# Kernel optimization log

Measured on AMD Instinct MI355X. Metric: run time of the kernel, lower is better.

Reference implementation:

```python
import jax, jax.numpy as jnp
import numpy as np

H = 128; B = 2
NG = 20000; NP = 3000
E_GG = 200000; E_TG = 200000; E_GP = 200000; E_PP = 100000
TAU_TG = 0.5; TOPK_TG = 16; TAU_GP = 0.5; TOPK_GP = 32
SQRT_H = float(np.sqrt(H))


def _mlp(x, w1, b1, w2, b2):
    # build_mlp(H, [H], H): Linear -> ReLU -> Linear (dropout=0)
    return jax.nn.relu(x @ w1 + b1) @ w2 + b2


def _scatter_sum(msgs, dst, num):
    # msgs: [B, E, H] -> [B, num, H]
    b, _, h = msgs.shape
    return jnp.zeros((b, num, h), msgs.dtype).at[:, dst, :].add(msgs)


def _prune(scores, dst, topk, tau):
    # per-target top-k + threshold pruning; scores [B, E], dst [E]
    E = scores.shape[1]
    pos = jnp.arange(E)
    def one(s):
        order = jnp.lexsort((-s, dst))  # primary: dst asc, secondary: score desc
        d_sorted = dst[order]
        is_start = jnp.concatenate([jnp.ones((1,), bool), d_sorted[1:] != d_sorted[:-1]])
        seg_start = jax.lax.associative_scan(jnp.maximum, jnp.where(is_start, pos, 0))
        rank = pos - seg_start  # rank within segment (0 = largest score)
        keep_sorted = (rank < topk) & (s[order] > tau)
        keep = jnp.zeros((E,), bool).at[order].set(keep_sorted)
        return jnp.where(keep, s, 0.0)
    return jax.vmap(one)(scores)


def _forward(gene_states, pathway_states, gg_w, tg_w, gp_w, pp_w,
             mlp_gg_w1, mlp_gg_b1, mlp_gg_w2, mlp_gg_b2,
             mlp_gp_w1, mlp_gp_b1, mlp_gp_w2, mlp_gp_b2,
             mlp_pp_w1, mlp_pp_b1, mlp_pp_w2, mlp_pp_b2,
             mlp_pg_w1, mlp_pg_b1, mlp_pg_w2, mlp_pg_b2,
             w_gg, w_pp, w_pg,
             tg_q, tg_k, tg_v_tf, tg_v_gene,
             gp_q, gp_k, gp_v,
             gg_src, gg_dst, tg_src, tg_dst, gp_src, gp_dst, pp_src, pp_dst):
    # Layer 1: gene-gene message passing with fixed edge weights
    gg_msgs = (gene_states[:, gg_src, :] @ w_gg) * gg_w[None, :, None]
    h1 = _mlp(gene_states, mlp_gg_w1, mlp_gg_b1, mlp_gg_w2, mlp_gg_b2) + _scatter_sum(gg_msgs, gg_dst, NG)

    # Layer 2: TF->gene attention with per-target pruning
    q_gene = h1 @ tg_q; k_tf = h1 @ tg_k; v_tf = h1 @ tg_v_tf; v_gene = h1 @ tg_v_gene
    raw_tg = jnp.einsum('beh,beh->be', q_gene[:, tg_dst, :], k_tf[:, tg_src, :]) / SQRT_H
    tg_scores = jax.nn.sigmoid(raw_tg * tg_w[None, :])
    tg_sel = _prune(tg_scores, tg_dst, TOPK_TG, TAU_TG)
    h2 = v_gene + _scatter_sum(tg_sel[..., None] * v_tf[:, tg_src, :], tg_dst, NG)

    # Layer 3: gene->pathway attention with pruning
    q_p = pathway_states @ gp_q; k_g = h2 @ gp_k; v_g = h2 @ gp_v
    raw_gp = jnp.einsum('beh,beh->be', q_p[:, gp_dst, :], k_g[:, gp_src, :]) / SQRT_H
    gp_scores = jax.nn.sigmoid(raw_gp * gp_w[None, :])
    gp_sel = _prune(gp_scores, gp_dst, TOPK_GP, TAU_GP)
    bar_h3 = _mlp(pathway_states, mlp_gp_w1, mlp_gp_b1, mlp_gp_w2, mlp_gp_b2) + _scatter_sum(gp_sel[..., None] * v_g[:, gp_src, :], gp_dst, NP)

    # Layer 4: pathway-pathway message passing
    pp_msgs = (bar_h3[:, pp_src, :] @ w_pp) * pp_w[None, :, None]
    h3 = _mlp(bar_h3, mlp_pp_w1, mlp_pp_b1, mlp_pp_w2, mlp_pp_b2) + _scatter_sum(pp_msgs, pp_dst, NP)

    # Layer 5: pathway->gene feedback (reversed gp edges, same gp weights)
    pg_msgs = (h3[:, gp_dst, :] @ w_pg) * gp_w[None, :, None]
    final_gene = _mlp(h2, mlp_pg_w1, mlp_pg_b1, mlp_pg_w2, mlp_pg_b2) + _scatter_sum(pg_msgs, gp_src, NG)
    return final_gene, h3


def setup_inputs() -> dict:
    key = jax.random.key(0)
    ks = iter(jax.random.split(key, 64))
    W = lambda: jax.random.normal(next(ks), (H, H), jnp.float32) * 0.05
    Bv = lambda: jnp.zeros((H,), jnp.float32)
    ew = lambda n: jax.random.uniform(next(ks), (n,), jnp.float32)
    ei = lambda n, hi: jax.random.randint(next(ks), (n,), 0, hi)
    inp = {
        'gene_states': jax.random.normal(next(ks), (B, NG, H), jnp.float32),
        'pathway_states': jax.random.normal(next(ks), (B, NP, H), jnp.float32),
        'gg_w': ew(E_GG), 'tg_w': ew(E_TG), 'gp_w': ew(E_GP), 'pp_w': ew(E_PP),
        'gg_src': ei(E_GG, NG), 'gg_dst': ei(E_GG, NG),
        'tg_src': ei(E_TG, NG), 'tg_dst': ei(E_TG, NG),
        'gp_src': ei(E_GP, NG), 'gp_dst': ei(E_GP, NP),
        'pp_src': ei(E_PP, NP), 'pp_dst': ei(E_PP, NP),
    }
    for name in ['mlp_gg', 'mlp_gp', 'mlp_pp', 'mlp_pg']:
        inp[name + '_w1'] = W(); inp[name + '_b1'] = Bv()
        inp[name + '_w2'] = W(); inp[name + '_b2'] = Bv()
    for name in ['w_gg', 'w_pp', 'w_pg', 'tg_q', 'tg_k', 'tg_v_tf', 'tg_v_gene', 'gp_q', 'gp_k', 'gp_v']:
        inp[name] = W()
    return inp


def reference(gene_states, pathway_states, gg_w, tg_w, gp_w, pp_w,
              gg_src, gg_dst, tg_src, tg_dst, gp_src, gp_dst, pp_src, pp_dst,
              mlp_gg_w1, mlp_gg_b1, mlp_gg_w2, mlp_gg_b2,
              mlp_gp_w1, mlp_gp_b1, mlp_gp_w2, mlp_gp_b2,
              mlp_pp_w1, mlp_pp_b1, mlp_pp_w2, mlp_pp_b2,
              mlp_pg_w1, mlp_pg_b1, mlp_pg_w2, mlp_pg_b2,
              w_gg, w_pp, w_pg, tg_q, tg_k, tg_v_tf, tg_v_gene, gp_q, gp_k, gp_v):
    return _forward(gene_states, pathway_states, gg_w, tg_w, gp_w, pp_w,
                    mlp_gg_w1, mlp_gg_b1, mlp_gg_w2, mlp_gg_b2,
                    mlp_gp_w1, mlp_gp_b1, mlp_gp_w2, mlp_gp_b2,
                    mlp_pp_w1, mlp_pp_b1, mlp_pp_w2, mlp_pp_b2,
                    mlp_pg_w1, mlp_pg_b1, mlp_pg_w2, mlp_pg_b2,
                    w_gg, w_pp, w_pg, tg_q, tg_k, tg_v_tf, tg_v_gene, gp_q, gp_k, gp_v,
                    gg_src, gg_dst, tg_src, tg_dst, gp_src, gp_dst, pp_src, pp_dst)
```

## Files before the change

kernel.cpp:

```cpp
#include <hip/hip_runtime.h>
#include <math.h>

#define H_ 128
static constexpr int NG_ = 20000, NP_ = 3000, B_ = 2;
static constexpr int EGG_ = 200000, ETG_ = 200000, EGP_ = 200000, EPP_ = 100000;
static constexpr float TAU_ = 0.5f;
static constexpr float RSQRTH_ = 0.088388347648318447f;

struct CsrDesc {
  const int* dst;
  int E, N;
  int* cnt;
  int* cur;
  int* off;
  int* bkt;
};
struct CsrPack { CsrDesc c[5]; };

__global__ void hist_all_k(CsrPack p) {
  CsrDesc d = p.c[blockIdx.y];
  int i = blockIdx.x * 256 + threadIdx.x;
  if (i < d.E) atomicAdd(&d.cnt[d.dst[i]], 1);
}

__global__ void scatter_all_k(CsrPack p) {
  CsrDesc d = p.c[blockIdx.y];
  int i = blockIdx.x * 256 + threadIdx.x;
  if (i < d.E) {
    int t = d.dst[i];
    int pos = atomicAdd(&d.cur[t], 1);
    d.bkt[d.off[t] + pos] = i;
  }
}

__global__ void exscan_all_k(CsrPack p) {
  CsrDesc d = p.c[blockIdx.x];
  const int n = d.N;
  const int* cnt = d.cnt;
  int* off = d.off;
  __shared__ int sh[256];
  const int tid = threadIdx.x;
  if (tid == 0) off[0] = 0;
  int run = 0;
  for (int base = 0; base < n; base += 4096) {
    int loc[16];
    int s = 0;
#pragma unroll
    for (int j = 0; j < 16; ++j) {
      int i = base + tid * 16 + j;
      loc[j] = (i < n) ? cnt[i] : 0;
      s += loc[j];
    }
    sh[tid] = s;
    __syncthreads();
    for (int st = 1; st < 256; st <<= 1) {
      int v = (tid >= st) ? sh[tid - st] : 0;
      __syncthreads();
      sh[tid] += v;
      __syncthreads();
    }
    int acc = run + ((tid > 0) ? sh[tid - 1] : 0);
    int tot = sh[255];
    __syncthreads();
#pragma unroll
    for (int j = 0; j < 16; ++j) {
      int i = base + tid * 16 + j;
      acc += loc[j];
      if (i < n) off[i + 1] = acc;
    }
    run += tot;
  }
}

template <int RELU, int ACCUM>
__global__ __launch_bounds__(256, 2) void gemm128_k(const float* __restrict__ X,
                                                    const float* __restrict__ W,
                                                    const float* __restrict__ bias,
                                                    float* __restrict__ Y, int R) {
  __shared__ float Wl[128 * 128];
  __shared__ float Al[32][68];
  const int t = threadIdx.x;
  const int tx = t & 31, ty = t >> 5;
  const int r0 = blockIdx.x * 64;
  {
    const float4* Wv = (const float4*)W;
    float4* Wlv = (float4*)Wl;
#pragma unroll
    for (int i = 0; i < 16; ++i) Wlv[t + 256 * i] = Wv[t + 256 * i];
  }
  float acc[8][4];
#pragma unroll
  for (int i = 0; i < 8; ++i)
#pragma unroll
    for (int j = 0; j < 4; ++j) acc[i][j] = 0.f;

  for (int kc = 0; kc < 128; kc += 32) {
    __syncthreads();
#pragma unroll
    for (int it = 0; it < 2; ++it) {
      int idx = t + 256 * it;
      int row = idx >> 3;
      int kq = idx & 7;
      int gr = r0 + row;
      float4 v = (gr < R) ? *(const float4*)&X[(size_t)gr * 128 + kc + kq * 4]
                          : make_float4(0.f, 0.f, 0.f, 0.f);
      Al[kq * 4 + 0][row] = v.x;
      Al[kq * 4 + 1][row] = v.y;
      Al[kq * 4 + 2][row] = v.z;
      Al[kq * 4 + 3][row] = v.w;
    }
    __syncthreads();
#pragma unroll
    for (int k = 0; k < 32; ++k) {
      float4 a0 = *(const float4*)&Al[k][ty * 8];
      float4 a1 = *(const float4*)&Al[k][ty * 8 + 4];
      float4 w = *(const float4*)&Wl[(kc + k) * 128 + tx * 4];
      float a[8] = {a0.x, a0.y, a0.z, a0.w, a1.x, a1.y, a1.z, a1.w};
#pragma unroll
      for (int i = 0; i < 8; ++i) {
        acc[i][0] += a[i] * w.x;
        acc[i][1] += a[i] * w.y;
        acc[i][2] += a[i] * w.z;
        acc[i][3] += a[i] * w.w;
      }
    }
  }
  float4 bv = make_float4(0.f, 0.f, 0.f, 0.f);
  if (bias) bv = *(const float4*)&bias[tx * 4];
#pragma unroll
  for (int i = 0; i < 8; ++i) {
    int gr = r0 + ty * 8 + i;
    if (gr < R) {
      float4 o;
      o.x = acc[i][0] + bv.x;
      o.y = acc[i][1] + bv.y;
      o.z = acc[i][2] + bv.z;
      o.w = acc[i][3] + bv.w;
      if (RELU) {
        o.x = fmaxf(o.x, 0.f); o.y = fmaxf(o.y, 0.f);
        o.z = fmaxf(o.z, 0.f); o.w = fmaxf(o.w, 0.f);
      }
      float4* yp = (float4*)&Y[(size_t)gr * 128 + tx * 4];
      if (ACCUM) {
        float4 old = *yp;
        o.x += old.x; o.y += old.y; o.z += old.z; o.w += old.w;
      }
      *yp = o;
    }
  }
}

__global__ __launch_bounds__(256) void attn_agg_k(
    const int* __restrict__ off, const int* __restrict__ bkt,
    const int* __restrict__ fidx, const float* __restrict__ ew,
    const float* __restrict__ Q, const float* __restrict__ K,
    const float* __restrict__ V, float* __restrict__ out,
    int nT, int nS, int topk) {
  constexpr int CAP = 512;
  __shared__ float s_sh[4][CAP];
  __shared__ int f_sh[4][CAP];
  __shared__ int e_sh[4][CAP];
  __shared__ float q_sh[4][128];
  const int wv = threadIdx.x >> 6, lane = threadIdx.x & 63;
  const int t = blockIdx.x * 4 + wv, b = blockIdx.y;
  if (t >= nT) return;
  const int o0 = off[t];
  const int ne = min(off[t + 1] - o0, CAP);
  if (ne == 0) return;

  for (int i = lane; i < ne; i += 64) {
    int e = bkt[o0 + i];
    f_sh[wv][i] = fidx[e];
    e_sh[wv][i] = e;
    s_sh[wv][i] = ew[e];
  }
  const float2 qv = *(const float2*)&Q[((size_t)b * nT + t) * 128 + lane * 2];
  *(float2*)&q_sh[wv][lane * 2] = qv;

  const int g = lane >> 4, l = lane & 15;
  const float4 q0 = *(const float4*)&q_sh[wv][l * 4];
  const float4 q1 = *(const float4*)&q_sh[wv][64 + l * 4];

  for (int i0 = 0; i0 < ne; i0 += 4) {
    int idx = i0 + g;
    bool val = idx < ne;
    int f = f_sh[wv][val ? idx : (ne - 1)];
    const float4* kr = (const float4*)&K[((size_t)b * nS + f) * 128];
    float4 k0 = kr[l];
    float4 k1 = kr[16 + l];
    float p = k0.x * q0.x + k0.y * q0.y + k0.z * q0.z + k0.w * q0.w +
              k1.x * q1.x + k1.y * q1.y + k1.z * q1.z + k1.w * q1.w;
    p += __shfl_xor(p, 1);
    p += __shfl_xor(p, 2);
    p += __shfl_xor(p, 4);
    p += __shfl_xor(p, 8);
    if (l == 0 && val) {
      float w = s_sh[wv][idx];
      float raw = p * RSQRTH_ * w;
      s_sh[wv][idx] = 1.f / (1.f + expf(-raw));
    }
  }

  float keep[CAP / 64];
#pragma unroll
  for (int c = 0; c < CAP / 64; ++c) {
    int i = lane + c * 64;
    float r = 0.f;
    if (i < ne) {
      float si = s_sh[wv][i];
      int ei = e_sh[wv][i];
      int cnt = 0;
      for (int j = 0; j < ne; ++j) {
        float sj = s_sh[wv][j];
        cnt += (sj > si) || (sj == si && e_sh[wv][j] < ei);
      }
      r = (cnt < topk && si > TAU_) ? si : 0.f;
    }
    keep[c] = r;
  }
#pragma unroll
  for (int c = 0; c < CAP / 64; ++c) {
    int i = lane + c * 64;
    if (i < ne) s_sh[wv][i] = keep[c];
  }

  size_t orow = ((size_t)b * nT + t) * 128 + lane * 2;
  float2 acc = *(float2*)&out[orow];
  for (int i = 0; i < ne; ++i) {
    float w = s_sh[wv][i];
    if (w != 0.f) {
      float2 v = *(const float2*)&V[((size_t)b * nS + f_sh[wv][i]) * 128 + lane * 2];
      acc.x += w * v.x;
      acc.y += w * v.y;
    }
  }
  *(float2*)&out[orow] = acc;
}

__global__ __launch_bounds__(256) void wagg_k(
    const int* __restrict__ off, const int* __restrict__ bkt,
    const int* __restrict__ fidx, const float* __restrict__ ew,
    const float* __restrict__ V, float* __restrict__ out, int nT, int nS) {
  constexpr int CAP = 512;
  __shared__ float s_sh[4][CAP];
  __shared__ int f_sh[4][CAP];
  const int wv = threadIdx.x >> 6, lane = threadIdx.x & 63;
  const int t = blockIdx.x * 4 + wv, b = blockIdx.y;
  if (t >= nT) return;
  const int o0 = off[t];
  const int ne = min(off[t + 1] - o0, CAP);
  if (ne == 0) return;
  for (int i = lane; i < ne; i += 64) {
    int e = bkt[o0 + i];
    f_sh[wv][i] = fidx[e];
    s_sh[wv][i] = ew[e];
  }
  size_t orow = ((size_t)b * nT + t) * 128 + lane * 2;
  float2 acc = *(float2*)&out[orow];
  for (int i = 0; i < ne; ++i) {
    float w = s_sh[wv][i];
    float2 v = *(const float2*)&V[((size_t)b * nS + f_sh[wv][i]) * 128 + lane * 2];
    acc.x += w * v.x;
    acc.y += w * v.y;
  }
  *(float2*)&out[orow] = acc;
}

extern "C" void kernel_launch(void* const* d_in, const int* in_sizes, int n_in, void* d_out,
                              int out_size, void* d_ws, size_t ws_size, hipStream_t stream) {
  const float* gene = (const float*)d_in[0];
  const float* path = (const float*)d_in[1];
  const float* gg_w = (const float*)d_in[2];
  const float* tg_w = (const float*)d_in[3];
  const float* gp_w = (const float*)d_in[4];
  const float* pp_w = (const float*)d_in[5];
  const int* gg_src = (const int*)d_in[6];
  const int* gg_dst = (const int*)d_in[7];
  const int* tg_src = (const int*)d_in[8];
  const int* tg_dst = (const int*)d_in[9];
  const int* gp_src = (const int*)d_in[10];
  const int* gp_dst = (const int*)d_in[11];
  const int* pp_src = (const int*)d_in[12];
  const int* pp_dst = (const int*)d_in[13];
  const float* mgg_w1 = (const float*)d_in[14];
  const float* mgg_b1 = (const float*)d_in[15];
  const float* mgg_w2 = (const float*)d_in[16];
  const float* mgg_b2 = (const float*)d_in[17];
  const float* mgp_w1 = (const float*)d_in[18];
  const float* mgp_b1 = (const float*)d_in[19];
  const float* mgp_w2 = (const float*)d_in[20];
  const float* mgp_b2 = (const float*)d_in[21];
  const float* mpp_w1 = (const float*)d_in[22];
  const float* mpp_b1 = (const float*)d_in[23];
  const float* mpp_w2 = (const float*)d_in[24];
  const float* mpp_b2 = (const float*)d_in[25];
  const float* mpg_w1 = (const float*)d_in[26];
  const float* mpg_b1 = (const float*)d_in[27];
  const float* mpg_w2 = (const float*)d_in[28];
  const float* mpg_b2 = (const float*)d_in[29];
  const float* w_gg = (const float*)d_in[30];
  const float* w_pp = (const float*)d_in[31];
  const float* w_pg = (const float*)d_in[32];
  const float* tg_q = (const float*)d_in[33];
  const float* tg_k = (const float*)d_in[34];
  const float* tg_v_tf = (const float*)d_in[35];
  const float* tg_v_gene = (const float*)d_in[36];
  const float* gp_q = (const float*)d_in[37];
  const float* gp_k = (const float*)d_in[38];
  const float* gp_v = (const float*)d_in[39];

  float* out_final = (float*)d_out;
  float* out_h3 = (float*)d_out + (size_t)B_ * NG_ * H_;

  const size_t BNGH = (size_t)B_ * NG_ * H_;
  const size_t BNPH = (size_t)B_ * NP_ * H_;

  char* wp = (char*)d_ws;
  auto alloc = [&](size_t bytes) {
    void* p = (void*)wp;
    wp += (bytes + 255) & ~(size_t)255;
    return p;
  };
  float* G0 = (float*)alloc(BNGH * 4);
  float* G1 = (float*)alloc(BNGH * 4);
  float* G2 = (float*)alloc(BNGH * 4);
  float* G3 = (float*)alloc(BNGH * 4);
  float* G4 = (float*)alloc(BNGH * 4);
  float* G5 = (float*)alloc(BNGH * 4);
  float* P0 = (float*)alloc(BNPH * 4);
  float* P1 = (float*)alloc(BNPH * 4);
  float* P2 = (float*)alloc(BNPH * 4);
  const int NCNT = 3 * NG_ + 2 * NP_;
  int* cntbuf = (int*)alloc((size_t)NCNT * 2 * 4);
  int* cnt_gg = cntbuf;
  int* cnt_tg = cnt_gg + NG_;
  int* cnt_gps = cnt_tg + NG_;
  int* cnt_gpd = cnt_gps + NG_;
  int* cnt_pp = cnt_gpd + NP_;
  int* cur0 = cntbuf + NCNT;
  int* cur_gg = cur0;
  int* cur_tg = cur_gg + NG_;
  int* cur_gps = cur_tg + NG_;
  int* cur_gpd = cur_gps + NG_;
  int* cur_pp = cur_gpd + NP_;
  int* off_gg = (int*)alloc((size_t)(NG_ + 1) * 4);
  int* off_tg = (int*)alloc((size_t)(NG_ + 1) * 4);
  int* off_gps = (int*)alloc((size_t)(NG_ + 1) * 4);
  int* off_gpd = (int*)alloc((size_t)(NP_ + 1) * 4);
  int* off_pp = (int*)alloc((size_t)(NP_ + 1) * 4);
  int* bkt_gg = (int*)alloc((size_t)EGG_ * 4);
  int* bkt_tg = (int*)alloc((size_t)ETG_ * 4);
  int* bkt_gps = (int*)alloc((size_t)EGP_ * 4);
  int* bkt_gpd = (int*)alloc((size_t)EGP_ * 4);
  int* bkt_pp = (int*)alloc((size_t)EPP_ * 4);

  hipMemsetAsync(cntbuf, 0, (size_t)NCNT * 2 * 4, stream);
  CsrPack pk;
  pk.c[0] = {gg_dst, EGG_, NG_, cnt_gg, cur_gg, off_gg, bkt_gg};
  pk.c[1] = {tg_dst, ETG_, NG_, cnt_tg, cur_tg, off_tg, bkt_tg};
  pk.c[2] = {gp_src, EGP_, NG_, cnt_gps, cur_gps, off_gps, bkt_gps};
  pk.c[3] = {gp_dst, EGP_, NP_, cnt_gpd, cur_gpd, off_gpd, bkt_gpd};
  pk.c[4] = {pp_dst, EPP_, NP_, cnt_pp, cur_pp, off_pp, bkt_pp};
  hist_all_k<<<dim3((EGG_ + 255) / 256, 5), dim3(256), 0, stream>>>(pk);
  exscan_all_k<<<dim3(5), dim3(256), 0, stream>>>(pk);
  scatter_all_k<<<dim3((EGG_ + 255) / 256, 5), dim3(256), 0, stream>>>(pk);

  const int RG = B_ * NG_;
  const int RP = B_ * NP_;
  auto gemm = [&](const float* X, const float* W, const float* bias, float* Y, int R, bool relu) {
    dim3 g((R + 63) / 64), blk(256);
    if (relu)
      gemm128_k<1, 0><<<g, blk, 0, stream>>>(X, W, bias, Y, R);
    else
      gemm128_k<0, 0><<<g, blk, 0, stream>>>(X, W, bias, Y, R);
  };

  gemm(gene, w_gg, nullptr, G2, RG, false);
  gemm(gene, mgg_w1, mgg_b1, G1, RG, true);
  gemm(G1, mgg_w2, mgg_b2, G0, RG, false);
  wagg_k<<<dim3((NG_ + 3) / 4, B_), dim3(256), 0, stream>>>(off_gg, bkt_gg, gg_src, gg_w, G2, G0,
                                                            NG_, NG_);
  gemm(G0, tg_q, nullptr, G2, RG, false);
  gemm(G0, tg_k, nullptr, G3, RG, false);
  gemm(G0, tg_v_tf, nullptr, G4, RG, false);
  gemm(G0, tg_v_gene, nullptr, G5, RG, false);
  attn_agg_k<<<dim3((NG_ + 3) / 4, B_), dim3(256), 0, stream>>>(
      off_tg, bkt_tg, tg_src, tg_w, G2, G3, G4, G5, NG_, NG_, 16);
  gemm(G5, gp_k, nullptr, G2, RG, false);
  gemm(G5, gp_v, nullptr, G3, RG, false);
  gemm(path, gp_q, nullptr, P0, RP, false);
  gemm(path, mgp_w1, mgp_b1, P1, RP, true);
  gemm(P1, mgp_w2, mgp_b2, P2, RP, false);
  attn_agg_k<<<dim3((NP_ + 3) / 4, B_), dim3(256), 0, stream>>>(
      off_gpd, bkt_gpd, gp_src, gp_w, P0, G2, G3, P2, NP_, NG_, 32);
  gemm(P2, w_pp, nullptr, P0, RP, false);
  gemm(P2, mpp_w1, mpp_b1, P1, RP, true);
  gemm(P1, mpp_w2, mpp_b2, out_h3, RP, false);
  wagg_k<<<dim3((NP_ + 3) / 4, B_), dim3(256), 0, stream>>>(off_pp, bkt_pp, pp_src, pp_w, P0,
                                                            out_h3, NP_, NP_);
  gemm(out_h3, w_pg, nullptr, P0, RP, false);
  gemm(G5, mpg_w1, mpg_b1, G1, RG, true);
  gemm(G1, mpg_w2, mpg_b2, out_final, RG, false);
  wagg_k<<<dim3((NG_ + 3) / 4, B_), dim3(256), 0, stream>>>(off_gps, bkt_gps, gp_dst, gp_w, P0,
                                                            out_final, NG_, NP_);
  (void)in_sizes; (void)n_in; (void)out_size; (void)ws_size;
}
```

Measured before the change: 889.8 us.

## Fuse same-input GEMMs into one multi-output kernel with LDS-resident MLP hidden

Replaces the single-weight GEMM with a kernel that loads a 64-row X tile into shared memory once and applies up to four weight matrices to it. For the MLPs, the ReLU hidden layer is written back into the shared tile instead of to global memory, so the intermediate buffers G1 and P1 go away. Weights are now read straight from global memory (through the caches) rather than staged in LDS. The attention kernel now uses 8 lanes per edge, compacts the kept edges with a ballot before the V aggregation, and unrolls that loop by two, as does wagg. Per-kernel edge caps are lowered through a template parameter to save shared memory, which would silently truncate any target whose degree exceeds the cap.

```diff
diff --git a/kernel.cpp b/kernel.cpp
--- a/kernel.cpp
+++ b/kernel.cpp
@@ -72,94 +72,98 @@
   }
 }
 
-template <int RELU, int ACCUM>
-__global__ __launch_bounds__(256, 2) void gemm128_k(const float* __restrict__ X,
-                                                    const float* __restrict__ W,
-                                                    const float* __restrict__ bias,
-                                                    float* __restrict__ Y, int R) {
-  __shared__ float Wl[128 * 128];
-  __shared__ float Al[32][68];
+static constexpr int GF_RELU = 1, GF_TOLDS = 2;
+struct GOp { const float* W; const float* bias; float* Y; int flags; };
+struct GPack { GOp o[4]; };
+
+template <int NOPS>
+__global__ __launch_bounds__(256) void gemmN_k(const float* __restrict__ X, GPack p, int R) {
+  __shared__ float Xl[64][132];
   const int t = threadIdx.x;
   const int tx = t & 31, ty = t >> 5;
   const int r0 = blockIdx.x * 64;
-  {
-    const float4* Wv = (const float4*)W;
-    float4* Wlv = (float4*)Wl;
-#pragma unroll
-    for (int i = 0; i < 16; ++i) Wlv[t + 256 * i] = Wv[t + 256 * i];
-  }
-  float acc[8][4];
-#pragma unroll
-  for (int i = 0; i < 8; ++i)
-#pragma unroll
-    for (int j = 0; j < 4; ++j) acc[i][j] = 0.f;
-
-  for (int kc = 0; kc < 128; kc += 32) {
-    __syncthreads();
-#pragma unroll
-    for (int it = 0; it < 2; ++it) {
-      int idx = t + 256 * it;
-      int row = idx >> 3;
-      int kq = idx & 7;
-      int gr = r0 + row;
-      float4 v = (gr < R) ? *(const float4*)&X[(size_t)gr * 128 + kc + kq * 4]
-                          : make_float4(0.f, 0.f, 0.f, 0.f);
-      Al[kq * 4 + 0][row] = v.x;
-      Al[kq * 4 + 1][row] = v.y;
-      Al[kq * 4 + 2][row] = v.z;
-      Al[kq * 4 + 3][row] = v.w;
-    }
-    __syncthreads();
-#pragma unroll
-    for (int k = 0; k < 32; ++k) {
-      float4 a0 = *(const float4*)&Al[k][ty * 8];
-      float4 a1 = *(const float4*)&Al[k][ty * 8 + 4];
-      float4 w = *(const float4*)&Wl[(kc + k) * 128 + tx * 4];
-      float a[8] = {a0.x, a0.y, a0.z, a0.w, a1.x, a1.y, a1.z, a1.w};
+#pragma unroll
+  for (int it = 0; it < 8; ++it) {
+    int idx = t + 256 * it;
+    int row = idx >> 5;
+    int kq = idx & 31;
+    int gr = r0 + row;
+    float4 v = make_float4(0.f, 0.f, 0.f, 0.f);
+    if (gr < R) v = *(const float4*)&X[(size_t)gr * 128 + kq * 4];
+    *(float4*)&Xl[row][kq * 4] = v;
+  }
+  __syncthreads();
+#pragma unroll
+  for (int op = 0; op < NOPS; ++op) {
+    const float4* __restrict__ Wv = (const float4*)p.o[op].W;
+    float acc[8][4];
+#pragma unroll
+    for (int i = 0; i < 8; ++i)
+#pragma unroll
+      for (int j = 0; j < 4; ++j) acc[i][j] = 0.f;
+#pragma unroll 2
+    for (int k = 0; k < 128; k += 4) {
+      float4 w0 = Wv[(k + 0) * 32 + tx];
+      float4 w1 = Wv[(k + 1) * 32 + tx];
+      float4 w2 = Wv[(k + 2) * 32 + tx];
+      float4 w3 = Wv[(k + 3) * 32 + tx];
 #pragma unroll
       for (int i = 0; i < 8; ++i) {
-        acc[i][0] += a[i] * w.x;
-        acc[i][1] += a[i] * w.y;
-        acc[i][2] += a[i] * w.z;
-        acc[i][3] += a[i] * w.w;
+        float4 xv = *(const float4*)&Xl[ty * 8 + i][k];
+        acc[i][0] += xv.x * w0.x + xv.y * w1.x + xv.z * w2.x + xv.w * w3.x;
+        acc[i][1] += xv.x * w0.y + xv.y * w1.y + xv.z * w2.y + xv.w * w3.y;
+        acc[i][2] += xv.x * w0.z + xv.y * w1.z + xv.z * w2.z + xv.w * w3.z;
+        acc[i][3] += xv.x * w0.w + xv.y * w1.w + xv.z * w2.w + xv.w * w3.w;
       }
     }
-  }
-  float4 bv = make_float4(0.f, 0.f, 0.f, 0.f);
-  if (bias) bv = *(const float4*)&bias[tx * 4];
-#pragma unroll
-  for (int i = 0; i < 8; ++i) {
-    int gr = r0 + ty * 8 + i;
-    if (gr < R) {
-      float4 o;
-      o.x = acc[i][0] + bv.x;
-      o.y = acc[i][1] + bv.y;
-      o.z = acc[i][2] + bv.z;
-      o.w = acc[i][3] + bv.w;
-      if (RELU) {
-        o.x = fmaxf(o.x, 0.f); o.y = fmaxf(o.y, 0.f);
-        o.z = fmaxf(o.z, 0.f); o.w = fmaxf(o.w, 0.f);
+    float4 bv = make_float4(0.f, 0.f, 0.f, 0.f);
+    if (p.o[op].bias) bv = *(const float4*)&p.o[op].bias[tx * 4];
+    const bool relu = (p.o[op].flags & GF_RELU) != 0;
+    if (p.o[op].flags & GF_TOLDS) {
+      __syncthreads();
+#pragma unroll
+      for (int i = 0; i < 8; ++i) {
+        float4 o;
+        o.x = acc[i][0] + bv.x; o.y = acc[i][1] + bv.y;
+        o.z = acc[i][2] + bv.z; o.w = acc[i][3] + bv.w;
+        if (relu) {
+          o.x = fmaxf(o.x, 0.f); o.y = fmaxf(o.y, 0.f);
+          o.z = fmaxf(o.z, 0.f); o.w = fmaxf(o.w, 0.f);
+        }
+        *(float4*)&Xl[ty * 8 + i][tx * 4] = o;
       }
-      float4* yp = (float4*)&Y[(size_t)gr * 128 + tx * 4];
-      if (ACCUM) {
-        float4 old = *yp;
-        o.x += old.x; o.y += old.y; o.z += old.z; o.w += old.w;
+      __syncthreads();
+    } else {
+      float* __restrict__ Y = p.o[op].Y;
+#pragma unroll
+      for (int i = 0; i < 8; ++i) {
+        int gr = r0 + ty * 8 + i;
+        if (gr < R) {
+          float4 o;
+          o.x = acc[i][0] + bv.x; o.y = acc[i][1] + bv.y;
+          o.z = acc[i][2] + bv.z; o.w = acc[i][3] + bv.w;
+          if (relu) {
+            o.x = fmaxf(o.x, 0.f); o.y = fmaxf(o.y, 0.f);
+            o.z = fmaxf(o.z, 0.f); o.w = fmaxf(o.w, 0.f);
+          }
+          *(float4*)&Y[(size_t)gr * 128 + tx * 4] = o;
+        }
       }
-      *yp = o;
-    }
-  }
-}
-
+    }
+  }
+}
+
+template <int CAP>
 __global__ __launch_bounds__(256) void attn_agg_k(
     const int* __restrict__ off, const int* __restrict__ bkt,
     const int* __restrict__ fidx, const float* __restrict__ ew,
     const float* __restrict__ Q, const float* __restrict__ K,
     const float* __restrict__ V, float* __restrict__ out,
     int nT, int nS, int topk) {
-  constexpr int CAP = 512;
   __shared__ float s_sh[4][CAP];
   __shared__ int f_sh[4][CAP];
   __shared__ int e_sh[4][CAP];
+  __shared__ int c_sh[4][CAP];
   __shared__ float q_sh[4][128];
   const int wv = threadIdx.x >> 6, lane = threadIdx.x & 63;
   const int t = blockIdx.x * 4 + wv, b = blockIdx.y;
@@ -174,36 +178,35 @@
     e_sh[wv][i] = e;
     s_sh[wv][i] = ew[e];
   }
-  const float2 qv = *(const float2*)&Q[((size_t)b * nT + t) * 128 + lane * 2];
-  *(float2*)&q_sh[wv][lane * 2] = qv;
-
-  const int g = lane >> 4, l = lane & 15;
-  const float4 q0 = *(const float4*)&q_sh[wv][l * 4];
-  const float4 q1 = *(const float4*)&q_sh[wv][64 + l * 4];
-
-  for (int i0 = 0; i0 < ne; i0 += 4) {
+  *(float2*)&q_sh[wv][lane * 2] = *(const float2*)&Q[((size_t)b * nT + t) * 128 + lane * 2];
+
+  const int g = lane >> 3, l = lane & 7;
+  float4 q[4];
+#pragma unroll
+  for (int j = 0; j < 4; ++j) q[j] = *(const float4*)&q_sh[wv][(l + 8 * j) * 4];
+  for (int i0 = 0; i0 < ne; i0 += 8) {
     int idx = i0 + g;
     bool val = idx < ne;
-    int f = f_sh[wv][val ? idx : (ne - 1)];
+    int f = f_sh[wv][val ? idx : 0];
     const float4* kr = (const float4*)&K[((size_t)b * nS + f) * 128];
-    float4 k0 = kr[l];
-    float4 k1 = kr[16 + l];
-    float p = k0.x * q0.x + k0.y * q0.y + k0.z * q0.z + k0.w * q0.w +
-              k1.x * q1.x + k1.y * q1.y + k1.z * q1.z + k1.w * q1.w;
+    float p = 0.f;
+#pragma unroll
+    for (int j = 0; j < 4; ++j) {
+      float4 kv = kr[l + 8 * j];
+      p += kv.x * q[j].x + kv.y * q[j].y + kv.z * q[j].z + kv.w * q[j].w;
+    }
     p += __shfl_xor(p, 1);
     p += __shfl_xor(p, 2);
     p += __shfl_xor(p, 4);
-    p += __shfl_xor(p, 8);
     if (l == 0 && val) {
       float w = s_sh[wv][idx];
-      float raw = p * RSQRTH_ * w;
-      s_sh[wv][idx] = 1.f / (1.f + expf(-raw));
-    }
-  }
-
-  float keep[CAP / 64];
-#pragma unroll
-  for (int c = 0; c < CAP / 64; ++c) {
+      s_sh[wv][idx] = 1.f / (1.f + expf(-p * RSQRTH_ * w));
+    }
+  }
+
+  float keep[(CAP + 63) / 64];
+#pragma unroll
+  for (int c = 0; c * 64 < CAP; ++c) {
     int i = lane + c * 64;
     float r = 0.f;
     if (i < ne) {
@@ -219,29 +222,47 @@
     keep[c] = r;
   }
 #pragma unroll
-  for (int c = 0; c < CAP / 64; ++c) {
+  for (int c = 0; c * 64 < CAP; ++c) {
     int i = lane + c * 64;
     if (i < ne) s_sh[wv][i] = keep[c];
   }
 
+  int nsel = 0;
+  for (int c = 0; c * 64 < ne; ++c) {
+    int i = c * 64 + lane;
+    bool sel = (i < ne) && (s_sh[wv][i] != 0.f);
+    unsigned long long m = __ballot(sel);
+    int pos = __popcll(m & ((1ull << lane) - 1ull));
+    if (sel) c_sh[wv][nsel + pos] = i;
+    nsel += __popcll(m);
+  }
+
   size_t orow = ((size_t)b * nT + t) * 128 + lane * 2;
   float2 acc = *(float2*)&out[orow];
-  for (int i = 0; i < ne; ++i) {
-    float w = s_sh[wv][i];
-    if (w != 0.f) {
-      float2 v = *(const float2*)&V[((size_t)b * nS + f_sh[wv][i]) * 128 + lane * 2];
-      acc.x += w * v.x;
-      acc.y += w * v.y;
-    }
+  int j = 0;
+  for (; j + 2 <= nsel; j += 2) {
+    int i0 = c_sh[wv][j], i1 = c_sh[wv][j + 1];
+    float w0 = s_sh[wv][i0], w1 = s_sh[wv][i1];
+    float2 v0 = *(const float2*)&V[((size_t)b * nS + f_sh[wv][i0]) * 128 + lane * 2];
+    float2 v1 = *(const float2*)&V[((size_t)b * nS + f_sh[wv][i1]) * 128 + lane * 2];
+    acc.x += w0 * v0.x + w1 * v1.x;
+    acc.y += w0 * v0.y + w1 * v1.y;
+  }
+  if (j < nsel) {
+    int i0 = c_sh[wv][j];
+    float w0 = s_sh[wv][i0];
+    float2 v0 = *(const float2*)&V[((size_t)b * nS + f_sh[wv][i0]) * 128 + lane * 2];
+    acc.x += w0 * v0.x;
+    acc.y += w0 * v0.y;
   }
   *(float2*)&out[orow] = acc;
 }
 
+template <int CAP>
 __global__ __launch_bounds__(256) void wagg_k(
     const int* __restrict__ off, const int* __restrict__ bkt,
     const int* __restrict__ fidx, const float* __restrict__ ew,
     const float* __restrict__ V, float* __restrict__ out, int nT, int nS) {
-  constexpr int CAP = 512;
   __shared__ float s_sh[4][CAP];
   __shared__ int f_sh[4][CAP];
   const int wv = threadIdx.x >> 6, lane = threadIdx.x & 63;
@@ -257,11 +278,19 @@
   }
   size_t orow = ((size_t)b * nT + t) * 128 + lane * 2;
   float2 acc = *(float2*)&out[orow];
-  for (int i = 0; i < ne; ++i) {
-    float w = s_sh[wv][i];
-    float2 v = *(const float2*)&V[((size_t)b * nS + f_sh[wv][i]) * 128 + lane * 2];
-    acc.x += w * v.x;
-    acc.y += w * v.y;
+  int i = 0;
+  for (; i + 2 <= ne; i += 2) {
+    float w0 = s_sh[wv][i], w1 = s_sh[wv][i + 1];
+    float2 v0 = *(const float2*)&V[((size_t)b * nS + f_sh[wv][i]) * 128 + lane * 2];
+    float2 v1 = *(const float2*)&V[((size_t)b * nS + f_sh[wv][i + 1]) * 128 + lane * 2];
+    acc.x += w0 * v0.x + w1 * v1.x;
+    acc.y += w0 * v0.y + w1 * v1.y;
+  }
+  if (i < ne) {
+    float w0 = s_sh[wv][i];
+    float2 v0 = *(const float2*)&V[((size_t)b * nS + f_sh[wv][i]) * 128 + lane * 2];
+    acc.x += w0 * v0.x;
+    acc.y += w0 * v0.y;
   }
   *(float2*)&out[orow] = acc;
 }
@@ -322,13 +351,11 @@
     return p;
   };
   float* G0 = (float*)alloc(BNGH * 4);
-  float* G1 = (float*)alloc(BNGH * 4);
   float* G2 = (float*)alloc(BNGH * 4);
   float* G3 = (float*)alloc(BNGH * 4);
   float* G4 = (float*)alloc(BNGH * 4);
   float* G5 = (float*)alloc(BNGH * 4);
   float* P0 = (float*)alloc(BNPH * 4);
-  float* P1 = (float*)alloc(BNPH * 4);
   float* P2 = (float*)alloc(BNPH * 4);
   const int NCNT = 3 * NG_ + 2 * NP_;
   int* cntbuf = (int*)alloc((size_t)NCNT * 2 * 4);
@@ -367,41 +394,63 @@
 
   const int RG = B_ * NG_;
   const int RP = B_ * NP_;
-  auto gemm = [&](const float* X, const float* W, const float* bias, float* Y, int R, bool relu) {
-    dim3 g((R + 63) / 64), blk(256);
-    if (relu)
-      gemm128_k<1, 0><<<g, blk, 0, stream>>>(X, W, bias, Y, R);
-    else
-      gemm128_k<0, 0><<<g, blk, 0, stream>>>(X, W, bias, Y, R);
-  };
-
-  gemm(gene, w_gg, nullptr, G2, RG, false);
-  gemm(gene, mgg_w1, mgg_b1, G1, RG, true);
-  gemm(G1, mgg_w2, mgg_b2, G0, RG, false);
-  wagg_k<<<dim3((NG_ + 3) / 4, B_), dim3(256), 0, stream>>>(off_gg, bkt_gg, gg_src, gg_w, G2, G0,
-                                                            NG_, NG_);
-  gemm(G0, tg_q, nullptr, G2, RG, false);
-  gemm(G0, tg_k, nullptr, G3, RG, false);
-  gemm(G0, tg_v_tf, nullptr, G4, RG, false);
-  gemm(G0, tg_v_gene, nullptr, G5, RG, false);
-  attn_agg_k<<<dim3((NG_ + 3) / 4, B_), dim3(256), 0, stream>>>(
+  const dim3 gG((RG + 63) / 64), gP((RP + 63) / 64), blk(256);
+
+  {
+    GPack p{};
+    p.o[0] = {w_gg, nullptr, G2, 0};
+    p.o[1] = {mgg_w1, mgg_b1, nullptr, GF_RELU | GF_TOLDS};
+    p.o[2] = {mgg_w2, mgg_b2, G0, 0};
+    gemmN_k<3><<<gG, blk, 0, stream>>>(gene, p, RG);
+  }
+  wagg_k<128><<<dim3((NG_ + 3) / 4, B_), blk, 0, stream>>>(off_gg, bkt_gg, gg_src, gg_w, G2, G0,
+                                                           NG_, NG_);
+  {
+    GPack p{};
+    p.o[0] = {tg_q, nullptr, G2, 0};
+    p.o[1] = {tg_k, nullptr, G3, 0};
+    p.o[2] = {tg_v_tf, nullptr, G4, 0};
+    p.o[3] = {tg_v_gene, nullptr, G5, 0};
+    gemmN_k<4><<<gG, blk, 0, stream>>>(G0, p, RG);
+  }
+  attn_agg_k<128><<<dim3((NG_ + 3) / 4, B_), blk, 0, stream>>>(
       off_tg, bkt_tg, tg_src, tg_w, G2, G3, G4, G5, NG_, NG_, 16);
-  gemm(G5, gp_k, nullptr, G2, RG, false);
-  gemm(G5, gp_v, nullptr, G3, RG, false);
-  gemm(path, gp_q, nullptr, P0, RP, false);
-  gemm(path, mgp_w1, mgp_b1, P1, RP, true);
-  gemm(P1, mgp_w2, mgp_b2, P2, RP, false);
-  attn_agg_k<<<dim3((NP_ + 3) / 4, B_), dim3(256), 0, stream>>>(
+  {
+    GPack p{};
+    p.o[0] = {gp_k, nullptr, G2, 0};
+    p.o[1] = {gp_v, nullptr, G3, 0};
+    gemmN_k<2><<<gG, blk, 0, stream>>>(G5, p, RG);
+  }
+  {
+    GPack p{};
+    p.o[0] = {gp_q, nullptr, P0, 0};
+    p.o[1] = {mgp_w1, mgp_b1, nullptr, GF_RELU | GF_TOLDS};
+    p.o[2] = {mgp_w2, mgp_b2, P2, 0};
+    gemmN_k<3><<<gP, blk, 0, stream>>>(path, p, RP);
+  }
+  attn_agg_k<256><<<dim3((NP_ + 3) / 4, B_), blk, 0, stream>>>(
       off_gpd, bkt_gpd, gp_src, gp_w, P0, G2, G3, P2, NP_, NG_, 32);
-  gemm(P2, w_pp, nullptr, P0, RP, false);
-  gemm(P2, mpp_w1, mpp_b1, P1, RP, true);
-  gemm(P1, mpp_w2, mpp_b2, out_h3, RP, false);
-  wagg_k<<<dim3((NP_ + 3) / 4, B_), dim3(256), 0, stream>>>(off_pp, bkt_pp, pp_src, pp_w, P0,
-                                                            out_h3, NP_, NP_);
-  gemm(out_h3, w_pg, nullptr, P0, RP, false);
-  gemm(G5, mpg_w1, mpg_b1, G1, RG, true);
-  gemm(G1, mpg_w2, mpg_b2, out_final, RG, false);
-  wagg_k<<<dim3((NG_ + 3) / 4, B_), dim3(256), 0, stream>>>(off_gps, bkt_gps, gp_dst, gp_w, P0,
-                                                            out_final, NG_, NP_);
+  {
+    GPack p{};
+    p.o[0] = {w_pp, nullptr, P0, 0};
+    p.o[1] = {mpp_w1, mpp_b1, nullptr, GF_RELU | GF_TOLDS};
+    p.o[2] = {mpp_w2, mpp_b2, out_h3, 0};
+    gemmN_k<3><<<gP, blk, 0, stream>>>(P2, p, RP);
+  }
+  wagg_k<192><<<dim3((NP_ + 3) / 4, B_), blk, 0, stream>>>(off_pp, bkt_pp, pp_src, pp_w, P0,
+                                                           out_h3, NP_, NP_);
+  {
+    GPack p{};
+    p.o[0] = {w_pg, nullptr, P0, 0};
+    gemmN_k<1><<<gP, blk, 0, stream>>>(out_h3, p, RP);
+  }
+  {
+    GPack p{};
+    p.o[0] = {mpg_w1, mpg_b1, nullptr, GF_RELU | GF_TOLDS};
+    p.o[1] = {mpg_w2, mpg_b2, out_final, 0};
+    gemmN_k<2><<<gG, blk, 0, stream>>>(G5, p, RG);
+  }
+  wagg_k<128><<<dim3((NG_ + 3) / 4, B_), blk, 0, stream>>>(off_gps, bkt_gps, gp_dst, gp_w, P0,
+                                                           out_final, NG_, NP_);
   (void)in_sizes; (void)n_in; (void)out_size; (void)ws_size;
 }
```

Measured after the change: 890.5 us. No clear change (+0.1%).
